# Kernel optimization log

Measured on AMD Instinct MI355X. Metric: run time of the kernel, lower is better.

Reference implementation:

```python
import jax, jax.numpy as jnp
import numpy as np

N = 384
NEG = jnp.float32(-1e30)


def setup_inputs() -> dict:
    key = jax.random.key(0)
    k1, k2, k3 = jax.random.split(key, 3)
    od = jax.random.uniform(k1, (N, N), dtype=jnp.float32) * 100.0  # OD demand (nn.Parameter in torch)
    adj = jax.random.randint(k2, (N, N), 0, 2, dtype=jnp.int32)     # binary adjacency
    dist = jax.random.uniform(k3, (N, N), dtype=jnp.float32) * 10.0 + 1.0  # free-flow times t0
    return {"od": od, "adj": adj, "dist": dist, "lambda_param": 1, "capacity": 500}


def _logit_assignment(od, adj, dist, lam):
    # Vectorized equivalent of the torch nested-loop logit assignment.
    # Paths have cutoff=2 edges: direct (o->d) and two-hop (o->k->d, k!=o, k!=d).
    n = od.shape[0]
    eye = jnp.eye(n, dtype=bool)
    # demand gated by od>0; diagonal OD pairs contribute no edge flow
    demand = jnp.where((od > 0) & ~eye, od, 0.0)
    A = (adj > 0) & ~eye  # usable directed edges (self-loops never on a simple path)
    # direct-path logits [o,d]
    l1 = jnp.where(A, -lam * dist, NEG)
    # two-hop path mask/times [o,k,d]; simple path => k!=o (in A), k!=d (in A), o!=d
    hop = A[:, :, None] & A[None, :, :] & (~eye)[:, None, :]
    t2 = dist[:, :, None] + dist[None, :, :]
    l2 = jnp.where(hop, -lam * t2, NEG)
    # stable softmax over {direct} u {all k} per OD pair
    m = jnp.maximum(l1, l2.max(axis=1))  # [o,d]
    e1 = jnp.where(A, jnp.exp(l1 - m), 0.0)
    e2 = jnp.where(hop, jnp.exp(l2 - m[:, None, :]), 0.0)
    Z = e1 + e2.sum(axis=1)  # [o,d]
    safe = Z > 0
    w = jnp.where(safe, demand / jnp.where(safe, Z, 1.0), 0.0)  # demand * (1/Z)
    # scatter assigned flow onto edges
    flows = w * e1                                       # direct edge (o,d)
    flows = flows + jnp.einsum('od,okd->ok', w, e2)      # first hop edge (o,k)
    flows = flows + jnp.einsum('od,okd->kd', w, e2)      # second hop edge (k,d)
    return flows


def reference(od, adj, dist, lambda_param, capacity):
    # max_iter=1 in the source, and the post-assignment BPR travel-time update is
    # under no_grad and only mutates G after the single assignment, so the returned
    # flow_results equals one logit assignment on the free-flow distances.
    lam = jnp.float32(lambda_param)
    return _logit_assignment(od, adj, dist, lam)
```

## Files before the change

### kernel.cpp

```cpp
#include <hip/hip_runtime.h>
#include <math.h>

#define NN 384
#define NT 24
#define NTILES (NT * NT)

typedef __attribute__((ext_vector_type(8))) short short8;
typedef __attribute__((ext_vector_type(4))) float v4f;

#define LOG2E 1.44269504088896340736f

__device__ __forceinline__ unsigned short f2bf(float f) {
    union { float f; unsigned u; } v; v.f = f;
    return (unsigned short)((v.u + 0x7FFFu + ((v.u >> 16) & 1u)) >> 16);
}
__device__ __forceinline__ float bf2f(unsigned short h) {
    union { unsigned u; float f; } v; v.u = ((unsigned)h) << 16;
    return v.f;
}

__global__ __launch_bounds__(64) void v_kernel(
    const float* __restrict__ dist, const int* __restrict__ adj,
    const float* __restrict__ od, const int* __restrict__ lam_ptr,
    unsigned short* __restrict__ P16, unsigned short* __restrict__ PT16,
    float* __restrict__ V32, unsigned short* __restrict__ V16,
    unsigned short* __restrict__ VT16)
{
    const int t = blockIdx.x;
    const int it = t / NT, jt = t % NT;
    const int i0 = it * 16, j0 = jt * 16;
    const int lane = threadIdx.x;
    const int col = lane & 15, quad = lane >> 4;
    const float lam = (float)(*lam_ptr);
    const float c = -lam * LOG2E;
    const int ir = i0 + col;
    const int jc = j0 + col;
    const bool diag = (it == jt);

    v4f acc = {0.f, 0.f, 0.f, 0.f};
#pragma unroll
    for (int k0 = 0; k0 < 12; ++k0) {
        const int kbase = k0 * 32 + quad * 8;
        float4 d0 = *(const float4*)(dist + ir * NN + kbase);
        float4 d1 = *(const float4*)(dist + ir * NN + kbase + 4);
        int4   a0 = *(const int4*)(adj + ir * NN + kbase);
        int4   a1 = *(const int4*)(adj + ir * NN + kbase + 4);
        float da[8] = {d0.x, d0.y, d0.z, d0.w, d1.x, d1.y, d1.z, d1.w};
        int   aa[8] = {a0.x, a0.y, a0.z, a0.w, a1.x, a1.y, a1.z, a1.w};
        short8 a, b;
#pragma unroll
        for (int e = 0; e < 8; ++e) {
            const int k = kbase + e;
            float pa = (aa[e] > 0 && ir != k) ? exp2f(c * da[e]) : 0.f;
            a[e] = (short)f2bf(pa);
            float db = dist[k * NN + jc];
            int   ab = adj[k * NN + jc];
            float pb = (ab > 0 && k != jc) ? exp2f(c * db) : 0.f;
            b[e] = (short)f2bf(pb);
        }
        if (diag) {
            *(short8*)(P16 + ir * NN + kbase) = a;
            *(short8*)(PT16 + jc * NN + kbase) = b;
        }
        acc = __builtin_amdgcn_mfma_f32_16x16x32_bf16(a, b, acc, 0, 0, 0);
    }

#pragma unroll
    for (int r = 0; r < 4; ++r) {
        const int i = i0 + quad * 4 + r, j = j0 + col;
        const int idx = i * NN + j;
        float p = (adj[idx] > 0 && i != j) ? exp2f(c * dist[idx]) : 0.f;
        p = bf2f(f2bf(p));
        const float denom = p + acc[r];
        const float o = od[idx];
        const float v = (i != j && o > 0.f && denom > 0.f) ? o / denom : 0.f;
        V32[idx] = v;
        const unsigned short h = f2bf(v);
        V16[idx] = h;
        VT16[j * NN + i] = h;
    }
}

__global__ __launch_bounds__(64) void flows_kernel(
    const unsigned short* __restrict__ P16, const unsigned short* __restrict__ PT16,
    const unsigned short* __restrict__ V16, const unsigned short* __restrict__ VT16,
    const float* __restrict__ V32, const int* __restrict__ adj,
    const float* __restrict__ dist, const int* __restrict__ lam_ptr,
    float* __restrict__ out)
{
    const int t = blockIdx.x;
    const int i0 = (t / NT) * 16, j0 = (t % NT) * 16;
    const int lane = threadIdx.x;
    const int col = lane & 15, quad = lane >> 4;
    v4f accW = {0.f, 0.f, 0.f, 0.f};
    v4f accU = {0.f, 0.f, 0.f, 0.f};
    const short8* aW = (const short8*)(V16 + (i0 + col) * NN + quad * 8);
    const short8* bW = (const short8*)(P16 + (j0 + col) * NN + quad * 8);
    const short8* aU = (const short8*)(PT16 + (i0 + col) * NN + quad * 8);
    const short8* bU = (const short8*)(VT16 + (j0 + col) * NN + quad * 8);
#pragma unroll
    for (int k0 = 0; k0 < 12; ++k0) {
        short8 a0 = aW[k0 * 4];
        short8 b0 = bW[k0 * 4];
        short8 a1 = aU[k0 * 4];
        short8 b1 = bU[k0 * 4];
        accW = __builtin_amdgcn_mfma_f32_16x16x32_bf16(a0, b0, accW, 0, 0, 0);
        accU = __builtin_amdgcn_mfma_f32_16x16x32_bf16(a1, b1, accU, 0, 0, 0);
    }
    const float lam = (float)(*lam_ptr);
    const float c = -lam * LOG2E;
#pragma unroll
    for (int r = 0; r < 4; ++r) {
        const int i = i0 + quad * 4 + r, j = j0 + col;
        const int idx = i * NN + j;
        const float p = (adj[idx] > 0 && i != j) ? exp2f(c * dist[idx]) : 0.f;
        out[idx] = p * (V32[idx] + accW[r] + accU[r]);
    }
}

extern "C" void kernel_launch(void* const* d_in, const int* in_sizes, int n_in,
                              void* d_out, int out_size, void* d_ws, size_t ws_size,
                              hipStream_t stream) {
    const float* od   = (const float*)d_in[0];
    const int*   adj  = (const int*)d_in[1];
    const float* dist = (const float*)d_in[2];
    const int*   lam  = (const int*)d_in[3];
    float* out = (float*)d_out;

    unsigned short* P16  = (unsigned short*)d_ws;
    unsigned short* PT16 = P16 + NN * NN;
    unsigned short* V16  = PT16 + NN * NN;
    unsigned short* VT16 = V16 + NN * NN;
    float*          V32  = (float*)(VT16 + NN * NN);

    v_kernel<<<NTILES, 64, 0, stream>>>(dist, adj, od, lam, P16, PT16, V32, V16, VT16);
    flows_kernel<<<NTILES, 64, 0, stream>>>(P16, PT16, V16, VT16, V32, adj, dist, lam, out);
}
```

Before: 84.11 us.

## Split K across four waves and stage bf16 exp tiles in LDS

Both kernels now run 256-thread blocks where four waves each handle a quarter of the K dimension with MFMA, then combine partial accumulators through shared memory. The first kernel also builds the bf16 exp(-lam*dist) row and column tiles cooperatively in LDS with coalesced loads, instead of each lane doing strided scalar column reads. It reuses the staged A tile for the direct-path term. The aim is more latency hiding and less uncoalesced global traffic, at the cost of extra syncs, a reduction step and LDS use per block.

```diff
diff --git a/kernel.cpp b/kernel.cpp
--- a/kernel.cpp
+++ b/kernel.cpp
@@ -4,9 +4,11 @@
 #define NN 384
 #define NT 24
 #define NTILES (NT * NT)
+#define LDSW 408
 
 typedef __attribute__((ext_vector_type(8))) short short8;
 typedef __attribute__((ext_vector_type(4))) float v4f;
+typedef __attribute__((ext_vector_type(4))) unsigned short ushort4v;
 
 #define LOG2E 1.44269504088896340736f
 
@@ -19,79 +21,116 @@
     return v.f;
 }
 
-__global__ __launch_bounds__(64) void v_kernel(
+__global__ __launch_bounds__(256) void v_build_kernel(
     const float* __restrict__ dist, const int* __restrict__ adj,
     const float* __restrict__ od, const int* __restrict__ lam_ptr,
     unsigned short* __restrict__ P16, unsigned short* __restrict__ PT16,
     float* __restrict__ V32, unsigned short* __restrict__ V16,
     unsigned short* __restrict__ VT16)
 {
+    __shared__ __align__(16) unsigned short As[16][LDSW];
+    __shared__ __align__(16) unsigned short Bs[16][LDSW];
+    __shared__ v4f Sp[3][64];
+
     const int t = blockIdx.x;
     const int it = t / NT, jt = t % NT;
     const int i0 = it * 16, j0 = jt * 16;
-    const int lane = threadIdx.x;
-    const int col = lane & 15, quad = lane >> 4;
+    const int tid = threadIdx.x;
     const float lam = (float)(*lam_ptr);
     const float c = -lam * LOG2E;
-    const int ir = i0 + col;
-    const int jc = j0 + col;
-    const bool diag = (it == jt);
 
+    {
+        const int r = tid >> 4;
+        const int cb = tid & 15;
+        const int gi = i0 + r;
+#pragma unroll
+        for (int s = 0; s < 6; ++s) {
+            const int c4 = (s * 16 + cb) * 4;
+            float4 d4 = *(const float4*)(dist + gi * NN + c4);
+            int4   a4 = *(const int4*)(adj + gi * NN + c4);
+            ushort4v h;
+            h[0] = (a4.x > 0 && gi != c4 + 0) ? f2bf(exp2f(c * d4.x)) : 0;
+            h[1] = (a4.y > 0 && gi != c4 + 1) ? f2bf(exp2f(c * d4.y)) : 0;
+            h[2] = (a4.z > 0 && gi != c4 + 2) ? f2bf(exp2f(c * d4.z)) : 0;
+            h[3] = (a4.w > 0 && gi != c4 + 3) ? f2bf(exp2f(c * d4.w)) : 0;
+            *(ushort4v*)&As[r][c4] = h;
+        }
+    }
+    {
+        const int c4 = (tid & 3) * 4;
+        const int r0 = tid >> 2;
+#pragma unroll
+        for (int p = 0; p < 6; ++p) {
+            const int rr = r0 + p * 64;
+            float4 d4 = *(const float4*)(dist + rr * NN + j0 + c4);
+            int4   a4 = *(const int4*)(adj + rr * NN + j0 + c4);
+            Bs[c4 + 0][rr] = (a4.x > 0 && rr != j0 + c4 + 0) ? f2bf(exp2f(c * d4.x)) : 0;
+            Bs[c4 + 1][rr] = (a4.y > 0 && rr != j0 + c4 + 1) ? f2bf(exp2f(c * d4.y)) : 0;
+            Bs[c4 + 2][rr] = (a4.z > 0 && rr != j0 + c4 + 2) ? f2bf(exp2f(c * d4.z)) : 0;
+            Bs[c4 + 3][rr] = (a4.w > 0 && rr != j0 + c4 + 3) ? f2bf(exp2f(c * d4.w)) : 0;
+        }
+    }
+    __syncthreads();
+
+    const int wave = tid >> 6, lane = tid & 63;
+    const int col = lane & 15, quad = lane >> 4;
     v4f acc = {0.f, 0.f, 0.f, 0.f};
 #pragma unroll
-    for (int k0 = 0; k0 < 12; ++k0) {
-        const int kbase = k0 * 32 + quad * 8;
-        float4 d0 = *(const float4*)(dist + ir * NN + kbase);
-        float4 d1 = *(const float4*)(dist + ir * NN + kbase + 4);
-        int4   a0 = *(const int4*)(adj + ir * NN + kbase);
-        int4   a1 = *(const int4*)(adj + ir * NN + kbase + 4);
-        float da[8] = {d0.x, d0.y, d0.z, d0.w, d1.x, d1.y, d1.z, d1.w};
-        int   aa[8] = {a0.x, a0.y, a0.z, a0.w, a1.x, a1.y, a1.z, a1.w};
-        short8 a, b;
-#pragma unroll
-        for (int e = 0; e < 8; ++e) {
-            const int k = kbase + e;
-            float pa = (aa[e] > 0 && ir != k) ? exp2f(c * da[e]) : 0.f;
-            a[e] = (short)f2bf(pa);
-            float db = dist[k * NN + jc];
-            int   ab = adj[k * NN + jc];
-            float pb = (ab > 0 && k != jc) ? exp2f(c * db) : 0.f;
-            b[e] = (short)f2bf(pb);
-        }
-        if (diag) {
-            *(short8*)(P16 + ir * NN + kbase) = a;
-            *(short8*)(PT16 + jc * NN + kbase) = b;
-        }
+    for (int kk = 0; kk < 3; ++kk) {
+        const int kbase = (wave * 3 + kk) * 32 + quad * 8;
+        short8 a = *(const short8*)&As[col][kbase];
+        short8 b = *(const short8*)&Bs[col][kbase];
         acc = __builtin_amdgcn_mfma_f32_16x16x32_bf16(a, b, acc, 0, 0, 0);
     }
+    if (wave) Sp[wave - 1][lane] = acc;
+    __syncthreads();
 
+    if (wave == 0) {
+        acc += Sp[0][lane];
+        acc += Sp[1][lane];
+        acc += Sp[2][lane];
 #pragma unroll
-    for (int r = 0; r < 4; ++r) {
-        const int i = i0 + quad * 4 + r, j = j0 + col;
-        const int idx = i * NN + j;
-        float p = (adj[idx] > 0 && i != j) ? exp2f(c * dist[idx]) : 0.f;
-        p = bf2f(f2bf(p));
-        const float denom = p + acc[r];
-        const float o = od[idx];
-        const float v = (i != j && o > 0.f && denom > 0.f) ? o / denom : 0.f;
-        V32[idx] = v;
-        const unsigned short h = f2bf(v);
-        V16[idx] = h;
-        VT16[j * NN + i] = h;
+        for (int r = 0; r < 4; ++r) {
+            const int i = i0 + quad * 4 + r, j = j0 + col;
+            const int idx = i * NN + j;
+            const float p = bf2f(As[quad * 4 + r][j]);
+            const float denom = p + acc[r];
+            const float o = od[idx];
+            const float v = (i != j && o > 0.f && denom > 0.f) ? o / denom : 0.f;
+            V32[idx] = v;
+            const unsigned short h = f2bf(v);
+            V16[idx] = h;
+            VT16[j * NN + i] = h;
+        }
+    }
+
+    if (it == jt) {
+        const int r = tid >> 4, cb = tid & 15;
+#pragma unroll
+        for (int s = 0; s < 6; ++s) {
+            const int c4 = (s * 16 + cb) * 4;
+            *(ushort4v*)(P16 + (i0 + r) * NN + c4) = *(const ushort4v*)&As[r][c4];
+            *(ushort4v*)(PT16 + (j0 + r) * NN + c4) = *(const ushort4v*)&Bs[r][c4];
+        }
     }
 }
 
-__global__ __launch_bounds__(64) void flows_kernel(
+__global__ __launch_bounds__(256) void flows_kernel(
     const unsigned short* __restrict__ P16, const unsigned short* __restrict__ PT16,
     const unsigned short* __restrict__ V16, const unsigned short* __restrict__ VT16,
     const float* __restrict__ V32, const int* __restrict__ adj,
     const float* __restrict__ dist, const int* __restrict__ lam_ptr,
     float* __restrict__ out)
 {
+    __shared__ v4f SpW[3][64];
+    __shared__ v4f SpU[3][64];
+
     const int t = blockIdx.x;
     const int i0 = (t / NT) * 16, j0 = (t % NT) * 16;
-    const int lane = threadIdx.x;
+    const int tid = threadIdx.x;
+    const int wave = tid >> 6, lane = tid & 63;
     const int col = lane & 15, quad = lane >> 4;
+
     v4f accW = {0.f, 0.f, 0.f, 0.f};
     v4f accU = {0.f, 0.f, 0.f, 0.f};
     const short8* aW = (const short8*)(V16 + (i0 + col) * NN + quad * 8);
@@ -99,22 +138,30 @@
     const short8* aU = (const short8*)(PT16 + (i0 + col) * NN + quad * 8);
     const short8* bU = (const short8*)(VT16 + (j0 + col) * NN + quad * 8);
 #pragma unroll
-    for (int k0 = 0; k0 < 12; ++k0) {
-        short8 a0 = aW[k0 * 4];
-        short8 b0 = bW[k0 * 4];
-        short8 a1 = aU[k0 * 4];
-        short8 b1 = bU[k0 * 4];
+    for (int kk = 0; kk < 3; ++kk) {
+        const int k4 = (wave * 3 + kk) * 4;
+        short8 a0 = aW[k4];
+        short8 b0 = bW[k4];
+        short8 a1 = aU[k4];
+        short8 b1 = bU[k4];
         accW = __builtin_amdgcn_mfma_f32_16x16x32_bf16(a0, b0, accW, 0, 0, 0);
         accU = __builtin_amdgcn_mfma_f32_16x16x32_bf16(a1, b1, accU, 0, 0, 0);
     }
-    const float lam = (float)(*lam_ptr);
-    const float c = -lam * LOG2E;
+    if (wave) { SpW[wave - 1][lane] = accW; SpU[wave - 1][lane] = accU; }
+    __syncthreads();
+
+    if (wave == 0) {
 #pragma unroll
-    for (int r = 0; r < 4; ++r) {
-        const int i = i0 + quad * 4 + r, j = j0 + col;
-        const int idx = i * NN + j;
-        const float p = (adj[idx] > 0 && i != j) ? exp2f(c * dist[idx]) : 0.f;
-        out[idx] = p * (V32[idx] + accW[r] + accU[r]);
+        for (int q = 0; q < 3; ++q) { accW += SpW[q][lane]; accU += SpU[q][lane]; }
+        const float lam = (float)(*lam_ptr);
+        const float c = -lam * LOG2E;
+#pragma unroll
+        for (int r = 0; r < 4; ++r) {
+            const int i = i0 + quad * 4 + r, j = j0 + col;
+            const int idx = i * NN + j;
+            const float p = (adj[idx] > 0 && i != j) ? exp2f(c * dist[idx]) : 0.f;
+            out[idx] = p * (V32[idx] + accW[r] + accU[r]);
+        }
     }
 }
 
@@ -133,6 +180,6 @@
     unsigned short* VT16 = V16 + NN * NN;
     float*          V32  = (float*)(VT16 + NN * NN);
 
-    v_kernel<<<NTILES, 64, 0, stream>>>(dist, adj, od, lam, P16, PT16, V32, V16, VT16);
-    flows_kernel<<<NTILES, 64, 0, stream>>>(P16, PT16, V16, VT16, V32, adj, dist, lam, out);
+    v_build_kernel<<<NTILES, 256, 0, stream>>>(dist, adj, od, lam, P16, PT16, V32, V16, VT16);
+    flows_kernel<<<NTILES, 256, 0, stream>>>(P16, PT16, V16, VT16, V32, adj, dist, lam, out);
 }
```

After: 79.98 us. 1.05x faster.

## Precompute bf16 P and its transpose in a separate kernel, widen MFMA tiles

Applied to the files above, without the earlier changes.

Adds a build kernel that computes the exp-weighted edge matrix P in bf16 once, plus its transpose through a shared-memory tile. The V kernel then reads P and PT directly instead of recomputing exp2 on strided uncoalesced dist/adj loads in every tile. The V and flows kernels move to 256-thread blocks where each wave computes a 16x32 tile, so each A fragment feeds two MFMAs. The cost is an extra kernel launch and a global round trip for P, and the grids shrink to 36 and 72 blocks, which leaves many CUs idle.

```diff
diff --git a/kernel.cpp b/kernel.cpp
--- a/kernel.cpp
+++ b/kernel.cpp
@@ -3,12 +3,11 @@
 
 #define NN 384
 #define NT 24
-#define NTILES (NT * NT)
+#define LOG2E 1.44269504088896340736f
 
 typedef __attribute__((ext_vector_type(8))) short short8;
 typedef __attribute__((ext_vector_type(4))) float v4f;
-
-#define LOG2E 1.44269504088896340736f
+typedef __attribute__((ext_vector_type(4))) unsigned short ushort4v;
 
 __device__ __forceinline__ unsigned short f2bf(float f) {
     union { float f; unsigned u; } v; v.f = f;
@@ -19,102 +18,138 @@
     return v.f;
 }
 
-__global__ __launch_bounds__(64) void v_kernel(
-    const float* __restrict__ dist, const int* __restrict__ adj,
-    const float* __restrict__ od, const int* __restrict__ lam_ptr,
-    unsigned short* __restrict__ P16, unsigned short* __restrict__ PT16,
+__global__ __launch_bounds__(256) void build_p_kernel(
+    const int* __restrict__ adj, const float* __restrict__ dist,
+    const int* __restrict__ lam_ptr,
+    unsigned short* __restrict__ P16, unsigned short* __restrict__ PT16)
+{
+    __shared__ unsigned int T[64][65];
+    const int b = blockIdx.x;
+    const int bi = (b / 6) * 64, bj = (b % 6) * 64;
+    const int tr = threadIdx.x >> 4;
+    const int tc = threadIdx.x & 15;
+    const float c = -(float)(*lam_ptr) * LOG2E;
+
+#pragma unroll
+    for (int s = 0; s < 4; ++s) {
+        const int gi = bi + s * 16 + tr;
+        const int gj = bj + tc * 4;
+        float4 d4 = *(const float4*)(dist + gi * NN + gj);
+        int4   a4 = *(const int4*)(adj + gi * NN + gj);
+        ushort4v h;
+        h[0] = (a4.x > 0 && gi != gj + 0) ? f2bf(exp2f(c * d4.x)) : 0;
+        h[1] = (a4.y > 0 && gi != gj + 1) ? f2bf(exp2f(c * d4.y)) : 0;
+        h[2] = (a4.z > 0 && gi != gj + 2) ? f2bf(exp2f(c * d4.z)) : 0;
+        h[3] = (a4.w > 0 && gi != gj + 3) ? f2bf(exp2f(c * d4.w)) : 0;
+        *(ushort4v*)(P16 + gi * NN + gj) = h;
+#pragma unroll
+        for (int e = 0; e < 4; ++e) T[tc * 4 + e][s * 16 + tr] = h[e];
+    }
+    __syncthreads();
+#pragma unroll
+    for (int s = 0; s < 4; ++s) {
+        const int prow = bj + s * 16 + tr;
+        const int pcol = bi + tc * 4;
+        ushort4v h;
+        h[0] = (unsigned short)T[s * 16 + tr][tc * 4 + 0];
+        h[1] = (unsigned short)T[s * 16 + tr][tc * 4 + 1];
+        h[2] = (unsigned short)T[s * 16 + tr][tc * 4 + 2];
+        h[3] = (unsigned short)T[s * 16 + tr][tc * 4 + 3];
+        *(ushort4v*)(PT16 + prow * NN + pcol) = h;
+    }
+}
+
+__global__ __launch_bounds__(256) void v_kernel(
+    const unsigned short* __restrict__ P16, const unsigned short* __restrict__ PT16,
+    const float* __restrict__ od,
     float* __restrict__ V32, unsigned short* __restrict__ V16,
     unsigned short* __restrict__ VT16)
 {
-    const int t = blockIdx.x;
-    const int it = t / NT, jt = t % NT;
-    const int i0 = it * 16, j0 = jt * 16;
-    const int lane = threadIdx.x;
+    const int tid = threadIdx.x;
+    const int wave = tid >> 6, lane = tid & 63;
+    const int sid = blockIdx.x * 4 + wave;
+    const int i0 = (sid / 12) * 16, j0 = (sid % 12) * 32;
     const int col = lane & 15, quad = lane >> 4;
-    const float lam = (float)(*lam_ptr);
-    const float c = -lam * LOG2E;
-    const int ir = i0 + col;
-    const int jc = j0 + col;
-    const bool diag = (it == jt);
 
-    v4f acc = {0.f, 0.f, 0.f, 0.f};
+    v4f acc0 = {0.f, 0.f, 0.f, 0.f};
+    v4f acc1 = {0.f, 0.f, 0.f, 0.f};
+    const short8* arow = (const short8*)(P16 + (i0 + col) * NN);
+    const short8* b0r  = (const short8*)(PT16 + (j0 + col) * NN);
+    const short8* b1r  = (const short8*)(PT16 + (j0 + 16 + col) * NN);
 #pragma unroll
     for (int k0 = 0; k0 < 12; ++k0) {
-        const int kbase = k0 * 32 + quad * 8;
-        float4 d0 = *(const float4*)(dist + ir * NN + kbase);
-        float4 d1 = *(const float4*)(dist + ir * NN + kbase + 4);
-        int4   a0 = *(const int4*)(adj + ir * NN + kbase);
-        int4   a1 = *(const int4*)(adj + ir * NN + kbase + 4);
-        float da[8] = {d0.x, d0.y, d0.z, d0.w, d1.x, d1.y, d1.z, d1.w};
-        int   aa[8] = {a0.x, a0.y, a0.z, a0.w, a1.x, a1.y, a1.z, a1.w};
-        short8 a, b;
+        const int o = k0 * 4 + quad;
+        short8 a  = arow[o];
+        short8 b0 = b0r[o];
+        short8 b1 = b1r[o];
+        acc0 = __builtin_amdgcn_mfma_f32_16x16x32_bf16(a, b0, acc0, 0, 0, 0);
+        acc1 = __builtin_amdgcn_mfma_f32_16x16x32_bf16(a, b1, acc1, 0, 0, 0);
+    }
 #pragma unroll
-        for (int e = 0; e < 8; ++e) {
-            const int k = kbase + e;
-            float pa = (aa[e] > 0 && ir != k) ? exp2f(c * da[e]) : 0.f;
-            a[e] = (short)f2bf(pa);
-            float db = dist[k * NN + jc];
-            int   ab = adj[k * NN + jc];
-            float pb = (ab > 0 && k != jc) ? exp2f(c * db) : 0.f;
-            b[e] = (short)f2bf(pb);
+    for (int t = 0; t < 2; ++t) {
+        v4f acc = t ? acc1 : acc0;
+#pragma unroll
+        for (int r = 0; r < 4; ++r) {
+            const int i = i0 + quad * 4 + r, j = j0 + t * 16 + col;
+            const int idx = i * NN + j;
+            const float denom = bf2f(P16[idx]) + acc[r];
+            const float o2 = od[idx];
+            const float v = (i != j && o2 > 0.f && denom > 0.f) ? o2 / denom : 0.f;
+            V32[idx] = v;
+            const unsigned short h = f2bf(v);
+            V16[idx] = h;
+            VT16[j * NN + i] = h;
         }
-        if (diag) {
-            *(short8*)(P16 + ir * NN + kbase) = a;
-            *(short8*)(PT16 + jc * NN + kbase) = b;
-        }
-        acc = __builtin_amdgcn_mfma_f32_16x16x32_bf16(a, b, acc, 0, 0, 0);
-    }
-
-#pragma unroll
-    for (int r = 0; r < 4; ++r) {
-        const int i = i0 + quad * 4 + r, j = j0 + col;
-        const int idx = i * NN + j;
-        float p = (adj[idx] > 0 && i != j) ? exp2f(c * dist[idx]) : 0.f;
-        p = bf2f(f2bf(p));
-        const float denom = p + acc[r];
-        const float o = od[idx];
-        const float v = (i != j && o > 0.f && denom > 0.f) ? o / denom : 0.f;
-        V32[idx] = v;
-        const unsigned short h = f2bf(v);
-        V16[idx] = h;
-        VT16[j * NN + i] = h;
     }
 }
 
-__global__ __launch_bounds__(64) void flows_kernel(
+__global__ __launch_bounds__(256) void flows_kernel(
     const unsigned short* __restrict__ P16, const unsigned short* __restrict__ PT16,
     const unsigned short* __restrict__ V16, const unsigned short* __restrict__ VT16,
     const float* __restrict__ V32, const int* __restrict__ adj,
     const float* __restrict__ dist, const int* __restrict__ lam_ptr,
     float* __restrict__ out)
 {
-    const int t = blockIdx.x;
-    const int i0 = (t / NT) * 16, j0 = (t % NT) * 16;
-    const int lane = threadIdx.x;
+    const int tid = threadIdx.x;
+    const int wave = tid >> 6, lane = tid & 63;
+    const int sid = blockIdx.x * 4 + wave;
+    const int i0 = (sid / 12) * 16, j0 = (sid % 12) * 32;
     const int col = lane & 15, quad = lane >> 4;
-    v4f accW = {0.f, 0.f, 0.f, 0.f};
-    v4f accU = {0.f, 0.f, 0.f, 0.f};
-    const short8* aW = (const short8*)(V16 + (i0 + col) * NN + quad * 8);
-    const short8* bW = (const short8*)(P16 + (j0 + col) * NN + quad * 8);
-    const short8* aU = (const short8*)(PT16 + (i0 + col) * NN + quad * 8);
-    const short8* bU = (const short8*)(VT16 + (j0 + col) * NN + quad * 8);
+
+    v4f accW0 = {0.f, 0.f, 0.f, 0.f}, accW1 = {0.f, 0.f, 0.f, 0.f};
+    v4f accU0 = {0.f, 0.f, 0.f, 0.f}, accU1 = {0.f, 0.f, 0.f, 0.f};
+    const short8* aWr  = (const short8*)(V16 + (i0 + col) * NN);
+    const short8* aUr  = (const short8*)(PT16 + (i0 + col) * NN);
+    const short8* bW0r = (const short8*)(P16 + (j0 + col) * NN);
+    const short8* bW1r = (const short8*)(P16 + (j0 + 16 + col) * NN);
+    const short8* bU0r = (const short8*)(VT16 + (j0 + col) * NN);
+    const short8* bU1r = (const short8*)(VT16 + (j0 + 16 + col) * NN);
 #pragma unroll
     for (int k0 = 0; k0 < 12; ++k0) {
-        short8 a0 = aW[k0 * 4];
-        short8 b0 = bW[k0 * 4];
-        short8 a1 = aU[k0 * 4];
-        short8 b1 = bU[k0 * 4];
-        accW = __builtin_amdgcn_mfma_f32_16x16x32_bf16(a0, b0, accW, 0, 0, 0);
-        accU = __builtin_amdgcn_mfma_f32_16x16x32_bf16(a1, b1, accU, 0, 0, 0);
+        const int o = k0 * 4 + quad;
+        short8 aW  = aWr[o];
+        short8 aU  = aUr[o];
+        short8 bW0 = bW0r[o];
+        short8 bW1 = bW1r[o];
+        short8 bU0 = bU0r[o];
+        short8 bU1 = bU1r[o];
+        accW0 = __builtin_amdgcn_mfma_f32_16x16x32_bf16(aW, bW0, accW0, 0, 0, 0);
+        accW1 = __builtin_amdgcn_mfma_f32_16x16x32_bf16(aW, bW1, accW1, 0, 0, 0);
+        accU0 = __builtin_amdgcn_mfma_f32_16x16x32_bf16(aU, bU0, accU0, 0, 0, 0);
+        accU1 = __builtin_amdgcn_mfma_f32_16x16x32_bf16(aU, bU1, accU1, 0, 0, 0);
     }
-    const float lam = (float)(*lam_ptr);
-    const float c = -lam * LOG2E;
+    const float c = -(float)(*lam_ptr) * LOG2E;
 #pragma unroll
-    for (int r = 0; r < 4; ++r) {
-        const int i = i0 + quad * 4 + r, j = j0 + col;
-        const int idx = i * NN + j;
-        const float p = (adj[idx] > 0 && i != j) ? exp2f(c * dist[idx]) : 0.f;
-        out[idx] = p * (V32[idx] + accW[r] + accU[r]);
+    for (int t = 0; t < 2; ++t) {
+        v4f accW = t ? accW1 : accW0;
+        v4f accU = t ? accU1 : accU0;
+#pragma unroll
+        for (int r = 0; r < 4; ++r) {
+            const int i = i0 + quad * 4 + r, j = j0 + t * 16 + col;
+            const int idx = i * NN + j;
+            const float p = (adj[idx] > 0 && i != j) ? exp2f(c * dist[idx]) : 0.f;
+            out[idx] = p * (V32[idx] + accW[r] + accU[r]);
+        }
     }
 }
 
@@ -133,6 +168,7 @@
     unsigned short* VT16 = V16 + NN * NN;
     float*          V32  = (float*)(VT16 + NN * NN);
 
-    v_kernel<<<NTILES, 64, 0, stream>>>(dist, adj, od, lam, P16, PT16, V32, V16, VT16);
-    flows_kernel<<<NTILES, 64, 0, stream>>>(P16, PT16, V16, VT16, V32, adj, dist, lam, out);
+    build_p_kernel<<<36, 256, 0, stream>>>(adj, dist, lam, P16, PT16);
+    v_kernel<<<72, 256, 0, stream>>>(P16, PT16, od, V32, V16, VT16);
+    flows_kernel<<<72, 256, 0, stream>>>(P16, PT16, V16, VT16, V32, adj, dist, lam, out);
 }
```

Measured after the change: 84.73 us. Within noise of the previous version (+0.7%).
